# Kernel tuning notes

Measured on AMD Instinct MI355X. Metric: run time of the kernel, lower is better.

## Reference

```python
import jax, jax.numpy as jnp
import numpy as np

N = 100_000       # nodes
E = 1_600_000     # edges
G = 128           # graphs in batch
RAW_ND, RAW_ED = 9, 3
ND, ED, H = 16, 2, 32  # node_dim, edge_dim, GAT hidden (heads=1)


def _p(key, shape, scale=0.1):
    return jax.random.normal(key, shape, dtype=jnp.float32) * scale


def setup_inputs() -> dict:
    key = jax.random.key(0)
    ks = jax.random.split(key, 32)
    inp = {
        "node_feat": jax.random.normal(ks[0], (N, RAW_ND), dtype=jnp.float32),
        "edge_index": jax.random.randint(ks[1], (2, E), 0, N, dtype=jnp.int64)
        if jax.config.jax_enable_x64 else jax.random.randint(ks[1], (2, E), 0, N).astype(jnp.int32),
        "edge_attr": jax.random.normal(ks[2], (E, RAW_ED), dtype=jnp.float32),
        "batch": jnp.sort(jax.random.randint(ks[3], (N,), 0, G)).astype(jnp.int32),
        # encoders
        "W_ne": _p(ks[4], (RAW_ND, ND)), "b_ne": jnp.zeros((ND,), jnp.float32),
        "W_ee": _p(ks[5], (RAW_ED, ED)), "b_ee": jnp.zeros((ED,), jnp.float32),
        # readout
        "W_l3": _p(ks[6], (3 * H, 1)), "b_l3": jnp.zeros((1,), jnp.float32),
    }
    dims_in = [ND, H, H]
    for i in range(3):
        k = jax.random.split(ks[7 + i], 6)
        inp[f"W{i}"] = _p(k[0], (dims_in[i], H))
        inp[f"as{i}"] = _p(k[1], (H,))
        inp[f"ad{i}"] = _p(k[2], (H,))
        inp[f"We{i}"] = _p(k[3], (ED, H))
        inp[f"ae{i}"] = _p(k[4], (H,))
        inp[f"bb{i}"] = jnp.zeros((H,), jnp.float32)
    return inp


def _segment_softmax(logits, seg, num_segments):
    m = jax.ops.segment_max(logits, seg, num_segments=num_segments)
    m = jnp.where(jnp.isfinite(m), m, 0.0)
    e = jnp.exp(logits - m[seg])
    s = jax.ops.segment_sum(e, seg, num_segments=num_segments)
    return e / (s[seg] + 1e-16)


def _gat(x, src, dst, ef, W, a_s, a_d, We, a_e, b):
    # PyG GATConv, heads=1, negative_slope=0.2
    h = x @ W                                   # [N', H]
    a_src = h @ a_s                             # [N']
    a_dst = h @ a_d
    a_edge = (ef @ We) @ a_e                    # [E']
    logits = jax.nn.leaky_relu(a_src[src] + a_dst[dst] + a_edge, 0.2)
    att = _segment_softmax(logits, dst, h.shape[0])
    out = jax.ops.segment_sum(h[src] * att[:, None], dst, num_segments=h.shape[0])
    return out + b


def reference(node_feat, edge_index, edge_attr, batch,
              W_ne, b_ne, W_ee, b_ee, W_l3, b_l3,
              W0, as0, ad0, We0, ae0, bb0,
              W1, as1, ad1, We1, ae1, bb1,
              W2, as2, ad2, We2, ae2, bb2):
    n = node_feat.shape[0]
    x = node_feat @ W_ne + b_ne                 # NodeEncoder -> [N,16]
    ef = edge_attr @ W_ee + b_ee                # EdgeEncoder -> [E,2]
    # add_self_loops=True with fill_value='mean' (PyG default when edge_dim set)
    loop = jnp.arange(n, dtype=edge_index.dtype)
    src = jnp.concatenate([edge_index[0], loop])
    dst = jnp.concatenate([edge_index[1], loop])
    ef_fill = jnp.broadcast_to(ef.mean(axis=0), (n, ef.shape[1]))
    ef_aug = jnp.concatenate([ef, ef_fill], axis=0)
    x1 = _gat(x, src, dst, ef_aug, W0, as0, ad0, We0, ae0, bb0)
    x2 = _gat(x1, src, dst, ef_aug, W1, as1, ad1, We1, ae1, bb1)
    x3 = _gat(x2, src, dst, ef_aug, W2, as2, ad2, We2, ae2, bb2)
    x_cat = jnp.concatenate([x1, x2, x3], axis=1)  # [N, 96]
    sums = jax.ops.segment_sum(x_cat, batch, num_segments=G)
    cnt = jax.ops.segment_sum(jnp.ones((n,), x_cat.dtype), batch, num_segments=G)
    pooled = sums / jnp.maximum(cnt, 1.0)[:, None]   # global mean pool [G,96]
    return pooled @ W_l3 + b_l3                      # [G,1]
```

## Files before the change

### kernel.cpp

```cpp
#include <hip/hip_runtime.h>
#include <hip/hip_fp16.h>


#define NBUCK_SHIFT 8
#define NBUCK_MAX 512
#define CAP 6144
#define SLF_BIT 0x00800000u

__global__ void k_pre(const int* __restrict__ ei1, int* __restrict__ bucket_cnt,
                      const int* __restrict__ batch, int* __restrict__ bounds,
                      const float* __restrict__ Wne, const float* __restrict__ bne,
                      const float* __restrict__ W0, float* __restrict__ wf,
                      int n, int e, int ep, int nbH) {
    int b = blockIdx.x, t = threadIdx.x;
    if (b < nbH) {
        __shared__ int lh[NBUCK_MAX];
        lh[t] = 0; lh[t + 256] = 0;
        __syncthreads();
        int base = b * 4096;
#pragma unroll
        for (int i = 0; i < 16; ++i) {
            int gid = base + i * 256 + t;
            if (gid < ep) {
                int d = (gid < e) ? ei1[gid] : gid - e;
                atomicAdd(&lh[d >> NBUCK_SHIFT], 1);
            }
        }
        __syncthreads();
        if (lh[t]) atomicAdd(&bucket_cnt[t], lh[t]);
        if (lh[t + 256]) atomicAdd(&bucket_cnt[t + 256], lh[t + 256]);
        return;
    }
    for (int i = t; i < 288; i += 256) {
        int m = i >> 5, j = i & 31;
        float a = 0.f;
        for (int k = 0; k < 16; ++k) a += Wne[m * 16 + k] * W0[k * 32 + j];
        wf[i] = a;
    }
    if (t < 32) {
        float a = 0.f;
        for (int k = 0; k < 16; ++k) a += bne[k] * W0[k * 32 + t];
        wf[288 + t] = a;
    }
    for (int g = t; g <= 128; g += 256) {
        if (g == 128) { bounds[128] = n; continue; }
        int lo = 0, hi = n;
        while (lo < hi) {
            int mid = (lo + hi) >> 1;
            if (batch[mid] < g) lo = mid + 1; else hi = mid;
        }
        bounds[g] = lo;
    }
}

__global__ void k_hproj0(const float* __restrict__ nf, const float* __restrict__ wf,
                         const float* __restrict__ as_, const float* __restrict__ ad_,
                         unsigned int* __restrict__ h2, float* __restrict__ asrc,
                         float* __restrict__ adst, int n) {
    int node = blockIdx.x * 8 + (threadIdx.x >> 5);
    int j = threadIdx.x & 31;
    if (node >= n) return;
    const float* xr = nf + node * 9;
    float acc = wf[288 + j];
#pragma unroll
    for (int m = 0; m < 9; ++m) acc += xr[m] * wf[m * 32 + j];
    float accp = __shfl_down(acc, 1, 32);
    if ((j & 1) == 0) {
        __half2 hh = __floats2half2_rn(acc, accp);
        h2[(size_t)node * 16 + (j >> 1)] = *reinterpret_cast<unsigned int*>(&hh);
    }
    float r1 = acc * as_[j], r2 = acc * ad_[j];
#pragma unroll
    for (int off = 16; off > 0; off >>= 1) {
        r1 += __shfl_xor(r1, off, 32);
        r2 += __shfl_xor(r2, off, 32);
    }
    if (j == 0) { asrc[node] = r1; adst[node] = r2; }
}

__device__ __forceinline__ float2 h2f2u(unsigned int hw) {
    __half2 hh = *reinterpret_cast<__half2*>(&hw);
    return make_float2(__low2float(hh), __high2float(hh));
}

__global__ void k_hproj(const unsigned int* __restrict__ xh, const float* __restrict__ W,
                        const float* __restrict__ as_, const float* __restrict__ ad_,
                        unsigned int* __restrict__ h2, float* __restrict__ asrc,
                        float* __restrict__ adst, int n) {
    __shared__ float sW[1024];
    for (int i = threadIdx.x; i < 1024; i += 256) sW[i] = W[i];
    __syncthreads();
    int node = blockIdx.x * 8 + (threadIdx.x >> 5);
    int j = threadIdx.x & 31;
    if (node >= n) return;
    const unsigned int* xr = xh + (size_t)node * 16;
    float acc = 0.f;
#pragma unroll
    for (int w = 0; w < 16; ++w) {
        float2 f = h2f2u(xr[w]);
        acc += f.x * sW[(2 * w) * 32 + j] + f.y * sW[(2 * w + 1) * 32 + j];
    }
    float accp = __shfl_down(acc, 1, 32);
    if ((j & 1) == 0) {
        __half2 hh = __floats2half2_rn(acc, accp);
        h2[(size_t)node * 16 + (j >> 1)] = *reinterpret_cast<unsigned int*>(&hh);
    }
    float r1 = acc * as_[j], r2 = acc * ad_[j];
#pragma unroll
    for (int off = 16; off > 0; off >>= 1) {
        r1 += __shfl_xor(r1, off, 32);
        r2 += __shfl_xor(r2, off, 32);
    }
    if (j == 0) { asrc[node] = r1; adst[node] = r2; }
}

__global__ void __launch_bounds__(512)
k_scan(const int* __restrict__ bucket_cnt, int* __restrict__ bucket_base,
       int* __restrict__ bcursor, int nbuck, int ep, int* __restrict__ rp, int n) {
    __shared__ int s[512];
    int t = threadIdx.x;
    int v = (t < nbuck) ? bucket_cnt[t] : 0;
    s[t] = v;
    __syncthreads();
    for (int o = 1; o < 512; o <<= 1) {
        int x = (t >= o) ? s[t - o] : 0;
        __syncthreads();
        s[t] += x;
        __syncthreads();
    }
    int ex = s[t] - v;
    if (t < nbuck) { bucket_base[t] = ex; bcursor[t] = ex; }
    if (t == 0) { bucket_base[nbuck] = ep; rp[n] = ep; }
}

__global__ void k_binB(const int* __restrict__ ei0, const int* __restrict__ ei1,
                       const float* __restrict__ ea, const float* __restrict__ We,
                       const float* __restrict__ be, int* __restrict__ bcursor,
                       uint2* __restrict__ st, float2* __restrict__ partial,
                       int e, int ep) {
    __shared__ int lh[NBUCK_MAX], lcur[NBUCK_MAX];
    int t = threadIdx.x;
    lh[t] = 0; lh[t + 256] = 0;
    __syncthreads();
    int base = blockIdx.x * 4096;
    unsigned int sd[16], fh[16];
    int bk[16];
    float w00 = We[0], w10 = We[2], w20 = We[4];
    float w01 = We[1], w11 = We[3], w21 = We[5];
    float b0 = be[0], b1 = be[1];
    float cs0 = 0.f, cs1 = 0.f;
#pragma unroll
    for (int i = 0; i < 16; ++i) {
        int gid = base + i * 256 + t;
        bk[i] = -1;
        if (gid < ep) {
            int s, d;
            if (gid < e) {
                s = ei0[gid]; d = ei1[gid];
                const float* r = ea + (size_t)gid * 3;
                float a0 = r[0], a1 = r[1], a2 = r[2];
                float f0 = a0 * w00 + a1 * w10 + a2 * w20 + b0;
                float f1 = a0 * w01 + a1 * w11 + a2 * w21 + b1;
                cs0 += f0; cs1 += f1;
                sd[i] = ((unsigned int)s << NBUCK_SHIFT) | (unsigned int)(d & 255);
                __half2 hh = __floats2half2_rn(f0, f1);
                fh[i] = *reinterpret_cast<unsigned int*>(&hh);
            } else {
                s = d = gid - e;
                sd[i] = 0x80000000u | ((unsigned int)s << NBUCK_SHIFT)
                      | (unsigned int)(d & 255);
                fh[i] = 0;
            }
            bk[i] = d >> NBUCK_SHIFT;
            atomicAdd(&lh[bk[i]], 1);
        }
    }
#pragma unroll
    for (int off = 32; off > 0; off >>= 1) {
        cs0 += __shfl_xor(cs0, off, 64);
        cs1 += __shfl_xor(cs1, off, 64);
    }
    if ((t & 63) == 0)
        partial[(blockIdx.x << 2) + (t >> 6)] = make_float2(cs0, cs1);
    __syncthreads();
    if (lh[t] > 0) lcur[t] = atomicAdd(&bcursor[t], lh[t]);
    if (lh[t + 256] > 0) lcur[t + 256] = atomicAdd(&bcursor[t + 256], lh[t + 256]);
    __syncthreads();
#pragma unroll
    for (int i = 0; i < 16; ++i) {
        if (bk[i] >= 0) {
            int pos = atomicAdd(&lcur[bk[i]], 1);
            st[pos] = make_uint2(sd[i], fh[i]);
        }
    }
}

__global__ void __launch_bounds__(512)
k_binC(const uint2* __restrict__ st, const int* __restrict__ bucket_base,
       int* __restrict__ rp, uint2* __restrict__ rec, int n, int nbuck,
       const float* __restrict__ We0, const float* __restrict__ ae0,
       const float* __restrict__ We1, const float* __restrict__ ae1,
       const float* __restrict__ We2, const float* __restrict__ ae2,
       const float2* __restrict__ partial, int nw, float einv,
       float* __restrict__ consts) {
    int k = blockIdx.x, t = threadIdx.x;
    if (k == nbuck) {
        __shared__ float r0[512], r1[512];
        float m0 = 0.f, m1 = 0.f;
        for (int i = t; i < nw; i += 512) {
            float2 v = partial[i];
            m0 += v.x; m1 += v.y;
        }
        r0[t] = m0; r1[t] = m1;
        __syncthreads();
        for (int o = 256; o > 0; o >>= 1) {
            if (t < o) { r0[t] += r0[t + o]; r1[t] += r1[t + o]; }
            __syncthreads();
        }
        if (t == 0) {
            float fm0 = r0[0] * einv, fm1 = r1[0] * einv;
            const float* We[3] = {We0, We1, We2};
            const float* ae[3] = {ae0, ae1, ae2};
            for (int l = 0; l < 3; ++l) {
                float c0 = 0.f, c1 = 0.f;
                for (int j = 0; j < 32; ++j) {
                    c0 += We[l][j] * ae[l][j];
                    c1 += We[l][32 + j] * ae[l][j];
                }
                consts[l * 2 + 0] = c0;
                consts[l * 2 + 1] = c1;
                consts[6 + l] = fm0 * c0 + fm1 * c1;
            }
        }
        return;
    }
    __shared__ int nh[256], ns[256];
    __shared__ uint2 rs[CAP];
    int s0 = bucket_base[k], s1 = bucket_base[k + 1];
    int cnt = s1 - s0;
    uint2 lv[12];
    if (t < 256) nh[t] = 0;
    __syncthreads();
#pragma unroll
    for (int u = 0; u < 12; ++u) {
        int i = s0 + u * 512 + t;
        if (i < s1) {
            uint2 v = st[i];
            lv[u] = v;
            atomicAdd(&nh[v.x & 255], 1);
        }
    }
    __syncthreads();
    if (t < 256) ns[t] = nh[t];
    __syncthreads();
    for (int o = 1; o < 256; o <<= 1) {
        int add = 0;
        if (t < 256 && t >= o) add = ns[t - o];
        __syncthreads();
        if (t < 256) ns[t] += add;
        __syncthreads();
    }
    int node0 = k << NBUCK_SHIFT;
    if (t < 256) {
        int startl = ns[t] - nh[t];
        if (node0 + t < n) rp[node0 + t] = s0 + startl;
        nh[t] = startl;
    }
    __syncthreads();
#pragma unroll
    for (int u = 0; u < 12; ++u) {
        int i = s0 + u * 512 + t;
        if (i < s1) {
            uint2 v = lv[u];
            int pos = atomicAdd(&nh[v.x & 255], 1);
            uint2 r = make_uint2(v.x >> NBUCK_SHIFT, v.y);
            if (pos < CAP) rs[pos] = r;
            else rec[s0 + pos] = r;
        }
    }
    __syncthreads();
    int m = cnt < CAP ? cnt : CAP;
    for (int i = t; i < m; i += 512)
        rec[s0 + i] = rs[i];
}

__device__ __forceinline__ float h2_get(const unsigned int* __restrict__ h2,
                                        int s, int word, bool hi) {
    unsigned int hw = h2[(size_t)s * 16 + word];
    __half2 hh = *reinterpret_cast<__half2*>(&hw);
    return hi ? __high2float(hh) : __low2float(hh);
}

template <bool STORE_X>
__global__ void k_agg(const int* __restrict__ rp, const uint2* __restrict__ rec,
                      const float* __restrict__ asrc, const float* __restrict__ adst,
                      const float* __restrict__ consts, const unsigned int* __restrict__ h2,
                      const float* __restrict__ bb, unsigned int* __restrict__ xout,
                      const float* __restrict__ wl3, float* __restrict__ vout,
                      int n, int layer) {
    int node = blockIdx.x * 8 + (threadIdx.x >> 5);
    int j = threadIdx.x & 31;
    if (node >= n) return;
    float c0 = consts[layer * 2], c1 = consts[layer * 2 + 1];
    float loopc = consts[6 + layer];
    int r0 = rp[node], r1 = rp[node + 1];
    float adn = adst[node];
    int word = j >> 1;
    bool hi = (j & 1) != 0;
    float acc = 0.f, psum = 0.f;
    for (int c = r0; c < r1; c += 32) {
        int i = c + j;
        float pe = 0.f; int s = 0;
        if (i < r1) {
            unsigned long long rv = __builtin_nontemporal_load(
                reinterpret_cast<const unsigned long long*>(rec + i));
            unsigned int sx = (unsigned int)(rv & 0xffffffffull);
            s = (int)(sx & 0x7fffffu);
            unsigned int fv = (unsigned int)(rv >> 32);
            __half2 hh = *reinterpret_cast<__half2*>(&fv);
            float ae = (sx & SLF_BIT) ? loopc
                     : (__low2float(hh) * c0 + __high2float(hh) * c1);
            float lg = asrc[s] + adn + ae;
            lg = lg > 0.f ? lg : 0.2f * lg;
            pe = __expf(lg);
        }
        psum += pe;
        int cnt = min(32, r1 - c);
        int t = 0;
        for (; t + 8 <= cnt; t += 8) {
            int s0 = __shfl(s, t, 32),     s1 = __shfl(s, t + 1, 32);
            int s2 = __shfl(s, t + 2, 32), s3 = __shfl(s, t + 3, 32);
            int s4 = __shfl(s, t + 4, 32), s5 = __shfl(s, t + 5, 32);
            int s6 = __shfl(s, t + 6, 32), s7 = __shfl(s, t + 7, 32);
            float p0 = __shfl(pe, t, 32),     p1 = __shfl(pe, t + 1, 32);
            float p2 = __shfl(pe, t + 2, 32), p3 = __shfl(pe, t + 3, 32);
            float p4 = __shfl(pe, t + 4, 32), p5 = __shfl(pe, t + 5, 32);
            float p6 = __shfl(pe, t + 6, 32), p7 = __shfl(pe, t + 7, 32);
            float h0 = h2_get(h2, s0, word, hi);
            float h1 = h2_get(h2, s1, word, hi);
            float h2v = h2_get(h2, s2, word, hi);
            float h3 = h2_get(h2, s3, word, hi);
            float h4 = h2_get(h2, s4, word, hi);
            float h5 = h2_get(h2, s5, word, hi);
            float h6 = h2_get(h2, s6, word, hi);
            float h7 = h2_get(h2, s7, word, hi);
            acc += p0 * h0; acc += p1 * h1; acc += p2 * h2v; acc += p3 * h3;
            acc += p4 * h4; acc += p5 * h5; acc += p6 * h6; acc += p7 * h7;
        }
        for (; t + 4 <= cnt; t += 4) {
            int s0 = __shfl(s, t, 32),     s1 = __shfl(s, t + 1, 32);
            int s2 = __shfl(s, t + 2, 32), s3 = __shfl(s, t + 3, 32);
            float p0 = __shfl(pe, t, 32),     p1 = __shfl(pe, t + 1, 32);
            float p2 = __shfl(pe, t + 2, 32), p3 = __shfl(pe, t + 3, 32);
            float h0 = h2_get(h2, s0, word, hi);
            float h1 = h2_get(h2, s1, word, hi);
            float h2v = h2_get(h2, s2, word, hi);
            float h3 = h2_get(h2, s3, word, hi);
            acc += p0 * h0; acc += p1 * h1; acc += p2 * h2v; acc += p3 * h3;
        }
        for (; t < cnt; ++t) {
            int st2 = __shfl(s, t, 32);
            float pt = __shfl(pe, t, 32);
            acc += pt * h2_get(h2, st2, word, hi);
        }
    }
#pragma unroll
    for (int off = 16; off > 0; off >>= 1) psum += __shfl_xor(psum, off, 32);
    float res = acc / (psum + 1e-16f) + bb[j];
    if (STORE_X) {
        float resp = __shfl_down(res, 1, 32);
        if ((j & 1) == 0) {
            __half2 hh = __floats2half2_rn(res, resp);
            xout[(size_t)node * 16 + (j >> 1)] = *reinterpret_cast<unsigned int*>(&hh);
        }
    }
    float v = res * wl3[j];
#pragma unroll
    for (int off = 16; off > 0; off >>= 1) v += __shfl_xor(v, off, 32);
    if (j == 0) vout[node] = v;
}

__global__ void k_dotv(const float* __restrict__ v0, const float* __restrict__ v1,
                       const float* __restrict__ v2, const int* __restrict__ bounds,
                       const float* __restrict__ bl3, float* __restrict__ out) {
    __shared__ float red[256];
    int g = blockIdx.x, t = threadIdx.x;
    int s0 = bounds[g], s1 = bounds[g + 1];
    float acc = 0.f;
    for (int i = s0 + t; i < s1; i += 256) acc += v0[i] + v1[i] + v2[i];
    red[t] = acc;
    __syncthreads();
    for (int o = 128; o > 0; o >>= 1) {
        if (t < o) red[t] += red[t + o];
        __syncthreads();
    }
    if (t == 0) {
        float c = (float)(s1 - s0);
        if (c < 1.f) c = 1.f;
        out[g] = red[0] / c + bl3[0];
    }
}

extern "C" void kernel_launch(void* const* d_in, const int* in_sizes, int n_in,
                              void* d_out, int out_size, void* d_ws, size_t ws_size,
                              hipStream_t stream) {
    (void)n_in; (void)out_size; (void)ws_size;
    const float* nf    = (const float*)d_in[0];
    const int*   ei    = (const int*)d_in[1];
    const float* ea    = (const float*)d_in[2];
    const int*   batch = (const int*)d_in[3];
    const float* W_ne  = (const float*)d_in[4];
    const float* b_ne  = (const float*)d_in[5];
    const float* W_ee  = (const float*)d_in[6];
    const float* b_ee  = (const float*)d_in[7];
    const float* W_l3  = (const float*)d_in[8];
    const float* b_l3  = (const float*)d_in[9];
    const float *Wl[3], *asl[3], *adl[3], *Wel[3], *ael[3], *bbl[3];
    for (int l = 0; l < 3; ++l) {
        Wl[l]  = (const float*)d_in[10 + 6 * l];
        asl[l] = (const float*)d_in[11 + 6 * l];
        adl[l] = (const float*)d_in[12 + 6 * l];
        Wel[l] = (const float*)d_in[13 + 6 * l];
        ael[l] = (const float*)d_in[14 + 6 * l];
        bbl[l] = (const float*)d_in[15 + 6 * l];
    }

    const int n  = in_sizes[3];
    const int e  = in_sizes[2] / 3;
    const int ep = e + n;
    const int* ei0 = ei;
    const int* ei1 = ei + e;
    const int nbuck = (n + 255) >> NBUCK_SHIFT;

    char* w = (char*)d_ws;
    size_t off = 0;
    auto alloc = [&](size_t b) { size_t o = off; off = (off + b + 255) & ~(size_t)255; return o; };
    unsigned int* x1h     = (unsigned int*)(w + alloc((size_t)n * 16 * 4));
    unsigned int* x2h     = (unsigned int*)(w + alloc((size_t)n * 16 * 4));
    unsigned int* h2a     = (unsigned int*)(w + alloc((size_t)n * 16 * 4));
    unsigned int* h2b     = (unsigned int*)(w + alloc((size_t)n * 16 * 4));
    float*        asrcA   = (float*)(w + alloc((size_t)n * 4));
    float*        adstA   = (float*)(w + alloc((size_t)n * 4));
    float*        asrcB   = (float*)(w + alloc((size_t)n * 4));
    float*        adstB   = (float*)(w + alloc((size_t)n * 4));
    float*        v0      = (float*)(w + alloc((size_t)n * 4));
    float*        v1      = (float*)(w + alloc((size_t)n * 4));
    float*        v2      = (float*)(w + alloc((size_t)n * 4));
    uint2*        st      = (uint2*)(w + alloc((size_t)ep * 8));
    uint2*        rec     = (uint2*)(w + alloc((size_t)ep * 8));
    int*          rp      = (int*)(w + alloc((size_t)(n + 1) * 4));
    int*          bcnt    = (int*)(w + alloc(NBUCK_MAX * 4));
    int*          bbase   = (int*)(w + alloc((NBUCK_MAX + 1) * 4));
    int*          bcur    = (int*)(w + alloc(NBUCK_MAX * 4));
    float2*       partial = (float2*)(w + alloc((size_t)8192 * 8));
    float*        consts  = (float*)(w + alloc(256));
    int*          bounds  = (int*)(w + alloc(129 * 4));
    float*        wfbuf   = (float*)(w + alloc(320 * 4));

    hipMemsetAsync(bcnt, 0, NBUCK_MAX * 4, stream);

    int nbH = (ep + 4095) / 4096;
    int nw  = nbH * 4;
    int nbN = (n + 7) / 8;

    k_pre<<<nbH + 1, 256, 0, stream>>>(ei1, bcnt, batch, bounds,
                                       W_ne, b_ne, Wl[0], wfbuf, n, e, ep, nbH);
    k_hproj0<<<nbN, 256, 0, stream>>>(nf, wfbuf, asl[0], adl[0],
                                      h2a, asrcA, adstA, n);
    k_scan<<<1, 512, 0, stream>>>(bcnt, bbase, bcur, nbuck, ep, rp, n);
    k_binB<<<nbH, 256, 0, stream>>>(ei0, ei1, ea, W_ee, b_ee, bcur, st,
                                    partial, e, ep);
    k_binC<<<nbuck + 1, 512, 0, stream>>>(st, bbase, rp, rec, n, nbuck,
                                          Wel[0], ael[0], Wel[1], ael[1],
                                          Wel[2], ael[2], partial, nw,
                                          1.0f / (float)e, consts);

    k_agg<true><<<nbN, 256, 0, stream>>>(rp, rec, asrcA, adstA, consts, h2a,
                                         bbl[0], x1h, W_l3 + 0, v0, n, 0);
    k_hproj<<<nbN, 256, 0, stream>>>(x1h, Wl[1], asl[1], adl[1], h2b, asrcB, adstB, n);
    k_agg<true><<<nbN, 256, 0, stream>>>(rp, rec, asrcB, adstB, consts, h2b,
                                         bbl[1], x2h, W_l3 + 32, v1, n, 1);
    k_hproj<<<nbN, 256, 0, stream>>>(x2h, Wl[2], asl[2], adl[2], h2a, asrcA, adstA, n);
    k_agg<false><<<nbN, 256, 0, stream>>>(rp, rec, asrcA, adstA, consts, h2a,
                                          bbl[2], nullptr, W_l3 + 64, v2, n, 2);
    k_dotv<<<128, 256, 0, stream>>>(v0, v1, v2, bounds, b_l3, (float*)d_out);
}
```

Measured before the change: 343.6 us.

## Restructure GAT aggregation so each lane loads 8-byte vectors for four edges in parallel

The aggregation loop now splits the 32 lanes into four groups of eight. Each group handles a different edge in the same step, and each lane loads a uint2, four fp16 features, instead of one half. This cuts the number of shuffles and load instructions per edge by about 4x and makes the gathers wider. In exchange it needs a cross-group shuffle reduction and a redistribution of the partial sums at the end. Tail edges beyond cnt rely on pe=0 and s=0 from the inactive lanes.

```diff
diff --git a/kernel.cpp b/kernel.cpp
--- a/kernel.cpp
+++ b/kernel.cpp
@@ -284,11 +284,19 @@
         rec[s0 + i] = rs[i];
 }
 
-__device__ __forceinline__ float h2_get(const unsigned int* __restrict__ h2,
-                                        int s, int word, bool hi) {
-    unsigned int hw = h2[(size_t)s * 16 + word];
-    __half2 hh = *reinterpret_cast<__half2*>(&hw);
-    return hi ? __high2float(hh) : __low2float(hh);
+__device__ __forceinline__ void agg_step(const unsigned int* __restrict__ h2,
+                                         int s, float pe, int t, int sub, int woff,
+                                         float& a0, float& a1, float& a2, float& a3) {
+    int idx = t + sub;
+    int s4 = __shfl(s, idx, 32);
+    float p4 = __shfl(pe, idx, 32);
+    uint2 hv = *reinterpret_cast<const uint2*>(h2 + ((s4 << 4) + woff));
+    __half2 hlo = *reinterpret_cast<__half2*>(&hv.x);
+    __half2 hhi = *reinterpret_cast<__half2*>(&hv.y);
+    a0 = fmaf(__low2float(hlo), p4, a0);
+    a1 = fmaf(__high2float(hlo), p4, a1);
+    a2 = fmaf(__low2float(hhi), p4, a2);
+    a3 = fmaf(__high2float(hhi), p4, a3);
 }
 
 template <bool STORE_X>
@@ -305,9 +313,10 @@
     float loopc = consts[6 + layer];
     int r0 = rp[node], r1 = rp[node + 1];
     float adn = adst[node];
-    int word = j >> 1;
-    bool hi = (j & 1) != 0;
-    float acc = 0.f, psum = 0.f;
+    int sub = j >> 3;
+    int woff = (j & 7) << 1;
+    float a0 = 0.f, a1 = 0.f, a2 = 0.f, a3 = 0.f;
+    float psum = 0.f;
     for (int c = r0; c < r1; c += 32) {
         int i = c + j;
         float pe = 0.f; int s = 0;
@@ -328,45 +337,25 @@
         int cnt = min(32, r1 - c);
         int t = 0;
         for (; t + 8 <= cnt; t += 8) {
-            int s0 = __shfl(s, t, 32),     s1 = __shfl(s, t + 1, 32);
-            int s2 = __shfl(s, t + 2, 32), s3 = __shfl(s, t + 3, 32);
-            int s4 = __shfl(s, t + 4, 32), s5 = __shfl(s, t + 5, 32);
-            int s6 = __shfl(s, t + 6, 32), s7 = __shfl(s, t + 7, 32);
-            float p0 = __shfl(pe, t, 32),     p1 = __shfl(pe, t + 1, 32);
-            float p2 = __shfl(pe, t + 2, 32), p3 = __shfl(pe, t + 3, 32);
-            float p4 = __shfl(pe, t + 4, 32), p5 = __shfl(pe, t + 5, 32);
-            float p6 = __shfl(pe, t + 6, 32), p7 = __shfl(pe, t + 7, 32);
-            float h0 = h2_get(h2, s0, word, hi);
-            float h1 = h2_get(h2, s1, word, hi);
-            float h2v = h2_get(h2, s2, word, hi);
-            float h3 = h2_get(h2, s3, word, hi);
-            float h4 = h2_get(h2, s4, word, hi);
-            float h5 = h2_get(h2, s5, word, hi);
-            float h6 = h2_get(h2, s6, word, hi);
-            float h7 = h2_get(h2, s7, word, hi);
-            acc += p0 * h0; acc += p1 * h1; acc += p2 * h2v; acc += p3 * h3;
-            acc += p4 * h4; acc += p5 * h5; acc += p6 * h6; acc += p7 * h7;
-        }
-        for (; t + 4 <= cnt; t += 4) {
-            int s0 = __shfl(s, t, 32),     s1 = __shfl(s, t + 1, 32);
-            int s2 = __shfl(s, t + 2, 32), s3 = __shfl(s, t + 3, 32);
-            float p0 = __shfl(pe, t, 32),     p1 = __shfl(pe, t + 1, 32);
-            float p2 = __shfl(pe, t + 2, 32), p3 = __shfl(pe, t + 3, 32);
-            float h0 = h2_get(h2, s0, word, hi);
-            float h1 = h2_get(h2, s1, word, hi);
-            float h2v = h2_get(h2, s2, word, hi);
-            float h3 = h2_get(h2, s3, word, hi);
-            acc += p0 * h0; acc += p1 * h1; acc += p2 * h2v; acc += p3 * h3;
-        }
-        for (; t < cnt; ++t) {
-            int st2 = __shfl(s, t, 32);
-            float pt = __shfl(pe, t, 32);
-            acc += pt * h2_get(h2, st2, word, hi);
-        }
-    }
+            agg_step(h2, s, pe, t, sub, woff, a0, a1, a2, a3);
+            agg_step(h2, s, pe, t + 4, sub, woff, a0, a1, a2, a3);
+        }
+        if (t < cnt) { agg_step(h2, s, pe, t, sub, woff, a0, a1, a2, a3); t += 4; }
+        if (t < cnt) { agg_step(h2, s, pe, t, sub, woff, a0, a1, a2, a3); }
+    }
+    a0 += __shfl_xor(a0, 8, 32);  a0 += __shfl_xor(a0, 16, 32);
+    a1 += __shfl_xor(a1, 8, 32);  a1 += __shfl_xor(a1, 16, 32);
+    a2 += __shfl_xor(a2, 8, 32);  a2 += __shfl_xor(a2, 16, 32);
+    a3 += __shfl_xor(a3, 8, 32);  a3 += __shfl_xor(a3, 16, 32);
 #pragma unroll
     for (int off = 16; off > 0; off >>= 1) psum += __shfl_xor(psum, off, 32);
-    float res = acc / (psum + 1e-16f) + bb[j];
+    float t0 = __shfl(a0, j >> 2, 32);
+    float t1 = __shfl(a1, j >> 2, 32);
+    float t2 = __shfl(a2, j >> 2, 32);
+    float t3 = __shfl(a3, j >> 2, 32);
+    int q = j & 3;
+    float accv = (q == 0) ? t0 : (q == 1) ? t1 : (q == 2) ? t2 : t3;
+    float res = accv / (psum + 1e-16f) + bb[j];
     if (STORE_X) {
         float resp = __shfl_down(res, 1, 32);
         if ((j & 1) == 0) {
```

After: 335.3 us. -2.4%, faster.
